# Kernel optimization log

Measured on AMD Instinct MI355X. Metric: run time of the kernel, lower is better.

## Reference

```python
import jax, jax.numpy as jnp
from jax import lax
import numpy as np

D_MODEL = 512
D_INNER = 1024   # expand=2 * d_model
D_STATE = 16
D_CONV = 4
DT_RANK = 32     # ceil(d_model/16)
B_SZ = 2
SEQ = 8192


def setup_inputs() -> dict:
    key = jax.random.key(0)
    ks = jax.random.split(key, 20)
    def n(k, shape, s=0.02):
        return jax.random.normal(k, shape, jnp.float32) * s
    inp = {
        "hidden_states": jax.random.normal(ks[0], (B_SZ, SEQ, D_MODEL), jnp.float32),
        "in_proj_w": n(ks[1], (2 * D_INNER, D_MODEL)),
        "out_proj_w": n(ks[2], (D_MODEL, D_INNER)),
    }
    for i, sfx in enumerate(["f", "r"]):
        b = 3 + i * 7
        inp[f"conv_w_{sfx}"] = n(ks[b], (D_INNER, 1, D_CONV), 0.1)
        inp[f"conv_b_{sfx}"] = n(ks[b + 1], (D_INNER,), 0.1)
        inp[f"xproj_w_{sfx}"] = n(ks[b + 2], (DT_RANK + 2 * D_STATE, D_INNER))
        inp[f"dtproj_w_{sfx}"] = n(ks[b + 3], (D_INNER, DT_RANK), 0.1)
        # softplus-inverse of dt_init ~0.01 (Mamba-style dt bias init)
        inp[f"dtproj_b_{sfx}"] = jnp.log(jnp.expm1(jnp.full((D_INNER,), 0.01, jnp.float32)))
        inp[f"A_log_{sfx}"] = jnp.log(jnp.tile(jnp.arange(1, D_STATE + 1, dtype=jnp.float32), (D_INNER, 1)))
        inp[f"D_{sfx}"] = jnp.ones((D_INNER,), jnp.float32)
    return inp


def _mamba(u, in_w, out_w, conv_w, conv_b, xproj_w, dt_w, dt_b, A_log, D_skip):
    # u: (B, L, D_MODEL)
    B, L, _ = u.shape
    xz = jnp.einsum('bld,ed->ble', u, in_w)          # (B, L, 2*D_INNER)
    x, z = jnp.split(xz, 2, axis=-1)
    # depthwise causal conv1d over time
    xt = lax.conv_general_dilated(
        x.transpose(0, 2, 1), conv_w, (1,), [(D_CONV - 1, 0)],
        dimension_numbers=('NCH', 'OIH', 'NCH'), feature_group_count=D_INNER)
    x = jax.nn.silu(xt.transpose(0, 2, 1) + conv_b)   # (B, L, D_INNER)
    # input-dependent dt, B, C
    xdbl = jnp.einsum('ble,fe->blf', x, xproj_w)      # (B, L, DT_RANK + 2*D_STATE)
    dt = xdbl[..., :DT_RANK]
    Bm = xdbl[..., DT_RANK:DT_RANK + D_STATE]         # (B, L, N)
    Cm = xdbl[..., DT_RANK + D_STATE:]                # (B, L, N)
    delta = jax.nn.softplus(jnp.einsum('blr,er->ble', dt, dt_w) + dt_b)  # (B, L, D_INNER)
    A = -jnp.exp(A_log)                               # (D_INNER, N)
    dA = jnp.exp(delta[..., None] * A)                # (B, L, D_INNER, N)
    dBu = delta[..., None] * Bm[:, :, None, :] * x[..., None]

    def step(h, inps):
        dA_t, dBu_t, C_t = inps
        h = dA_t * h + dBu_t                          # (B, D_INNER, N)
        return h, jnp.einsum('ben,bn->be', h, C_t)

    h0 = jnp.zeros((B, D_INNER, D_STATE), u.dtype)
    _, ys = lax.scan(step, h0, (dA.transpose(1, 0, 2, 3),
                                dBu.transpose(1, 0, 2, 3),
                                Cm.transpose(1, 0, 2)))
    y = ys.transpose(1, 0, 2) + x * D_skip            # (B, L, D_INNER)
    y = y * jax.nn.silu(z)
    return jnp.einsum('ble,de->bld', y, out_w)


def reference(hidden_states, in_proj_w, out_proj_w,
              conv_w_f, conv_b_f, xproj_w_f, dtproj_w_f, dtproj_b_f, A_log_f, D_f,
              conv_w_r, conv_b_r, xproj_w_r, dtproj_w_r, dtproj_b_r, A_log_r, D_r):
    out = _mamba(hidden_states, in_proj_w, out_proj_w,
                 conv_w_f, conv_b_f, xproj_w_f, dtproj_w_f, dtproj_b_f, A_log_f, D_f)
    out_rev = _mamba(hidden_states[:, ::-1], in_proj_w, out_proj_w,
                     conv_w_r, conv_b_r, xproj_w_r, dtproj_w_r, dtproj_b_r, A_log_r, D_r)[:, ::-1]
    return out + out_rev
```

## Files before the change

### kernel.cpp

```cpp
#include <hip/hip_runtime.h>
#include <hip/hip_bf16.h>
#include <math.h>

#define B_SZ 2
#define SEQ  8192
#define DM   512
#define DI   1024
#define DS   16
#define DTR  32
#define M_TOT (B_SZ*SEQ)
#define LOG2E 1.44269504088896f
#define NCHAN  (4*DI*DS)
#define NG     (4*DI)
#define CLT    8

typedef __attribute__((ext_vector_type(8))) short bf16x8;
typedef __attribute__((ext_vector_type(4))) float f32x4;
typedef __attribute__((ext_vector_type(2))) float f32x2;
typedef unsigned short u16;

__device__ __forceinline__ float bf2f(u16 u){
  union { unsigned u; float f; } v; v.u = ((unsigned)u) << 16; return v.f;
}
__device__ __forceinline__ u16 f2bf(float f){
  union { float f; unsigned u; } v; v.f = f;
  unsigned r = v.u + 0x7FFFu + ((v.u >> 16) & 1u);
  return (u16)(r >> 16);
}
__device__ __forceinline__ float silu_f(float x){ return x / (1.f + __expf(-x)); }
__device__ __forceinline__ float softplus_f(float x){
  return (x > 15.f) ? x : __logf(1.f + __expf(x));
}
__device__ __forceinline__ float fexp2(float x){ return __builtin_amdgcn_exp2f(x); }

__device__ __forceinline__ void dA_generic(float d, const float* A2, float* dAv){
  #pragma unroll
  for (int n = 0; n < DS; n++) dAv[n] = fexp2(A2[n] * d);
}

__global__ __launch_bounds__(256) void cvt_k(
    const float* __restrict__ s, u16* __restrict__ d)
{
  const size_t i = (size_t)blockIdx.x * 256 + threadIdx.x;
  const float4 a = ((const float4*)s)[i * 2];
  const float4 b = ((const float4*)s)[i * 2 + 1];
  union { uint4 v; u16 h[8]; } o;
  o.h[0] = f2bf(a.x); o.h[1] = f2bf(a.y); o.h[2] = f2bf(a.z); o.h[3] = f2bf(a.w);
  o.h[4] = f2bf(b.x); o.h[5] = f2bf(b.y); o.h[6] = f2bf(b.z); o.h[7] = f2bf(b.w);
  ((uint4*)d)[i] = o.v;
}

#define WU_INW  131072
#define WU_XW   8192
#define WU_DTW  4096
#define WU_OUTW 65536
#define WU_TOT  (WU_INW + 2*WU_XW + 2*WU_DTW + WU_OUTW)
__global__ __launch_bounds__(256) void cvtw_k(
    const float* __restrict__ inw, const float* __restrict__ xwf,
    const float* __restrict__ xwr, const float* __restrict__ dtwf,
    const float* __restrict__ dtwr, const float* __restrict__ outw,
    u16* __restrict__ dst)
{
  int i = blockIdx.x * 256 + threadIdx.x;
  const float* s;
  int base = 0;
  if (i < WU_INW) { s = inw; }
  else if ((i -= WU_INW) < WU_XW) { s = xwf; base = WU_INW; }
  else if ((i -= WU_XW) < WU_XW)  { s = xwr; base = WU_INW + WU_XW; }
  else if ((i -= WU_XW) < WU_DTW) { s = dtwf; base = WU_INW + 2*WU_XW; }
  else if ((i -= WU_DTW) < WU_DTW){ s = dtwr; base = WU_INW + 2*WU_XW + WU_DTW; }
  else { i -= WU_DTW; s = outw; base = WU_INW + 2*WU_XW + 2*WU_DTW; }
  const float4 a = ((const float4*)s)[i * 2];
  const float4 b = ((const float4*)s)[i * 2 + 1];
  union { uint4 v; u16 h[8]; } o;
  o.h[0] = f2bf(a.x); o.h[1] = f2bf(a.y); o.h[2] = f2bf(a.z); o.h[3] = f2bf(a.w);
  o.h[4] = f2bf(b.x); o.h[5] = f2bf(b.y); o.h[6] = f2bf(b.z); o.h[7] = f2bf(b.w);
  ((uint4*)(dst))[base + i] = o.v;
}

template<int BN, int BK, int EPI, bool DUAL>
__global__ __launch_bounds__(256) void gemm_k(
    const u16* __restrict__ Ap,  const u16* __restrict__ Ap2, int lda,
    const u16* __restrict__ Bw,  const u16* __restrict__ Bw2, int K,
    void* __restrict__ out0, void* __restrict__ out02,
    void* __restrict__ out1, void* __restrict__ out12,
    const float* __restrict__ bias, const float* __restrict__ bias2, int ldo)
{
  constexpr int BM = 128;
  constexpr int NSLOT = BK / 8;
  constexpr int RPI   = 512 / BK;
  __shared__ __align__(16) u16 As[BM * BK];
  __shared__ __align__(16) u16 Bs[BN * BK];
  const int tid  = threadIdx.x;
  const int lane = tid & 63, wid = tid >> 6;
  const int mt = blockIdx.x, nt = blockIdx.y;
  const int z  = DUAL ? blockIdx.z : 0;
  const u16* A = z ? Ap2 : Ap;
  const u16* W = z ? Bw2 : Bw;
  void* o0 = z ? out02 : out0;
  void* o1 = z ? out12 : out1;
  const float* bi = z ? bias2 : bias;

  constexpr int FM = (BN == 128) ? 4 : 2;
  const int wm = (BN == 128) ? ((wid >> 1) * 64) : (wid * 32);
  const int wn = (BN == 128) ? ((wid & 1) * 64) : 0;

  f32x4 acc[FM][4];
  #pragma unroll
  for (int i = 0; i < FM; i++)
    #pragma unroll
    for (int j = 0; j < 4; j++)
      acc[i][j] = (f32x4){0.f, 0.f, 0.f, 0.f};

  const int sr   = lane / NSLOT;
  const int slot = lane % NSLOT;
  const int skey = (BK == 32) ? ((sr >> 1) & 3) : (sr & 7);
  const int sc   = (slot ^ skey) * 8;

  for (int k0 = 0; k0 < K; k0 += BK) {
    #pragma unroll
    for (int j = 0; j < BM / RPI / 4; j++) {
      const int chunk = wid * (BM / RPI / 4) + j;
      const u16* src = A + (size_t)(mt * BM + chunk * RPI + sr) * lda + (k0 + sc);
      __builtin_amdgcn_global_load_lds(
          (const __attribute__((address_space(1))) void*)src,
          (__attribute__((address_space(3))) void*)(As + chunk * 512), 16, 0, 0);
    }
    #pragma unroll
    for (int j = 0; j < BN / RPI / 4; j++) {
      const int chunk = wid * (BN / RPI / 4) + j;
      const u16* src = W + (size_t)(nt * BN + chunk * RPI + sr) * K + (k0 + sc);
      __builtin_amdgcn_global_load_lds(
          (const __attribute__((address_space(1))) void*)src,
          (__attribute__((address_space(3))) void*)(Bs + chunk * 512), 16, 0, 0);
    }
    __syncthreads();

    const int row  = lane & 15;
    const int rkey = (BK == 32) ? ((row >> 1) & 3) : (row & 7);
    #pragma unroll
    for (int kh = 0; kh < BK / 32; kh++) {
      const int sl = (kh * 4 + (lane >> 4)) ^ rkey;
      bf16x8 af[FM], bfr[4];
      #pragma unroll
      for (int i = 0; i < FM; i++)
        af[i] = *(const bf16x8*)&As[(wm + i * 16 + row) * BK + sl * 8];
      #pragma unroll
      for (int j = 0; j < 4; j++)
        bfr[j] = *(const bf16x8*)&Bs[(wn + j * 16 + row) * BK + sl * 8];
      #pragma unroll
      for (int i = 0; i < FM; i++)
        #pragma unroll
        for (int j = 0; j < 4; j++)
          acc[i][j] = __builtin_amdgcn_mfma_f32_16x16x32_bf16(af[i], bfr[j], acc[i][j], 0, 0, 0);
    }
    __syncthreads();
  }

  const int rb4 = (lane >> 4) * 4, col = lane & 15;
  #pragma unroll
  for (int i = 0; i < FM; i++) {
    #pragma unroll
    for (int j = 0; j < 4; j++) {
      #pragma unroll
      for (int r = 0; r < 4; r++) {
        const int m = mt * BM + wm + i * 16 + rb4 + r;
        const int n = nt * BN + wn + j * 16 + col;
        const float v = acc[i][j][r];
        if (EPI == 0) {
          if (n < DI) ((u16*)o0)[(size_t)m * DI + n] = f2bf(v);
          else        ((u16*)out1)[(size_t)m * DI + (n - DI)] = f2bf(silu_f(v));
        } else if (EPI == 1) {
          ((u16*)o0)[(size_t)m * ldo + n] = f2bf(v);
          if (n >= 32) ((float*)o1)[(size_t)m * 32 + (n - 32)] = v;
        } else if (EPI == 2) {
          ((u16*)o0)[(size_t)m * ldo + n] = f2bf(softplus_f(v + bi[n]));
        } else {
          ((float*)o0)[(size_t)m * ldo + n] = v;
        }
      }
    }
  }
}

__global__ __launch_bounds__(256) void conv2_k(
    const u16* __restrict__ xpre,
    const float* __restrict__ wf, const float* __restrict__ bf_,
    const float* __restrict__ wr, const float* __restrict__ br_,
    u16* __restrict__ xf, u16* __restrict__ xr)
{
  const int tid  = threadIdx.x;
  const int et   = tid & 127;
  const int lsub = tid >> 7;
  const int e0 = et * 8;
  const int b  = blockIdx.y;
  const int l0 = (blockIdx.x * 2 + lsub) * CLT;
  const size_t base = (size_t)b * SEQ * DI + e0;

  float4 wf4[8], wr4[8];
  float  bfv[8], brv[8];
  #pragma unroll
  for (int j = 0; j < 8; j++) {
    wf4[j] = *(const float4*)(wf + (e0 + j) * 4);
    wr4[j] = *(const float4*)(wr + (e0 + j) * 4);
    bfv[j] = bf_[e0 + j];
    brv[j] = br_[e0 + j];
  }

  float c0[8], c1[8], c2[8];
  auto loadv = [&](int l, float* dst) {
    if (l < 0 || l >= SEQ) {
      #pragma unroll
      for (int j = 0; j < 8; j++) dst[j] = 0.f;
      return;
    }
    union { uint4 v; u16 s[8]; } t;
    t.v = *(const uint4*)(xpre + base + (size_t)l * DI);
    #pragma unroll
    for (int j = 0; j < 8; j++) dst[j] = bf2f(t.s[j]);
  };
  loadv(l0 - 3, c0); loadv(l0 - 2, c1); loadv(l0 - 1, c2);

  #pragma unroll
  for (int i = 0; i < CLT + 3; i++) {
    const int l = l0 + i;
    float cn[8];
    loadv(l, cn);
    if (i < CLT) {
      union { uint4 v; u16 s[8]; } o;
      #pragma unroll
      for (int j = 0; j < 8; j++) {
        const float v = bfv[j] + wf4[j].x * c0[j] + wf4[j].y * c1[j]
                               + wf4[j].z * c2[j] + wf4[j].w * cn[j];
        o.s[j] = f2bf(silu_f(v));
      }
      *(uint4*)(xf + base + (size_t)l * DI) = o.v;
    }
    if (i >= 3) {
      const int lr = l - 3;
      union { uint4 v; u16 s[8]; } o;
      #pragma unroll
      for (int j = 0; j < 8; j++) {
        const float v = brv[j] + wr4[j].w * c0[j] + wr4[j].z * c1[j]
                               + wr4[j].y * c2[j] + wr4[j].x * cn[j];
        o.s[j] = f2bf(silu_f(v));
      }
      *(uint4*)(xr + base + (size_t)(SEQ - 1 - lr) * DI) = o.v;
    }
    #pragma unroll
    for (int j = 0; j < 8; j++) { c0[j] = c1[j]; c1[j] = c2[j]; c2[j] = cn[j]; }
  }
}

__device__ __forceinline__ bool a_check(const float* Al, int e, float& A20){
  float A2[DS];
  #pragma unroll
  for (int n = 0; n < DS; n++) A2[n] = -__expf(Al[e * DS + n]) * LOG2E;
  A20 = A2[0];
  bool st = true;
  #pragma unroll
  for (int n = 1; n < DS; n++)
    st = st && (fabsf(A2[n] - (float)(n + 1) * A20) <= 1e-3f * fabsf(A2[n]));
  return st;
}

template<int CT_>
__global__ __launch_bounds__(128) void scanA2_k(
    const float* __restrict__ bcf, const float* __restrict__ bcr,
    const u16* __restrict__ xf_,   const u16* __restrict__ xr_,
    const float* __restrict__ Alf, const float* __restrict__ Alr,
    const u16* __restrict__ df_,   const u16* __restrict__ dr_,
    float* __restrict__ sumdP, float* __restrict__ bP)
{
  const int e = blockIdx.x * 128 + threadIdx.x;
  const int c = blockIdx.y;
  const int dir = blockIdx.z >> 1, b = blockIdx.z & 1;
  const float* bc = dir ? bcr : bcf;
  const u16* x    = dir ? xr_ : xf_;
  const float* Al = dir ? Alr : Alf;
  const u16* dpre = dir ? dr_ : df_;

  float A20;
  const bool structured = a_check(Al, e, A20);

  float sumd = 0.f;
  const size_t m0 = (size_t)b * SEQ + (size_t)c * CT_;
  const int g = (dir * 2 + b) * DI + e;
  const size_t cb = (size_t)c * NCHAN + (size_t)g * DS;

  if (structured) {
    f32x2 h2[8];
    #pragma unroll
    for (int k = 0; k < 8; k++) h2[k] = (f32x2){0.f, 0.f};
    #pragma unroll 2
    for (int t = 0; t < CT_; t++) {
      const size_t m = m0 + t;
      const float d  = bf2f(dpre[m * DI + e]);
      const float xv = bf2f(x[m * DI + e]);
      const float dbx = d * xv;
      sumd += d;
      const f32x4* bp = (const f32x4*)(bc + m * 32);
      const f32x4 b0 = bp[0], b1 = bp[1], b2 = bp[2], b3 = bp[3];
      const float q = fexp2(A20 * d), q2 = q * q, q4 = q2 * q2, q8 = q4 * q4;
      const f32x2 q2v = (f32x2){q2, q2}, q4v = (f32x2){q4, q4}, q8v = (f32x2){q8, q8};
      const f32x2 dbx2 = (f32x2){dbx, dbx};
      const f32x2 p0 = (f32x2){q, q2};
      const f32x2 p1 = p0 * q2v, p2 = p0 * q4v, p3 = p1 * q4v;
      const f32x2 p4 = p0 * q8v, p5 = p1 * q8v, p6 = p2 * q8v, p7 = p3 * q8v;
      h2[0] = p0 * h2[0] + dbx2 * (f32x2){b0[0], b0[1]};
      h2[1] = p1 * h2[1] + dbx2 * (f32x2){b0[2], b0[3]};
      h2[2] = p2 * h2[2] + dbx2 * (f32x2){b1[0], b1[1]};
      h2[3] = p3 * h2[3] + dbx2 * (f32x2){b1[2], b1[3]};
      h2[4] = p4 * h2[4] + dbx2 * (f32x2){b2[0], b2[1]};
      h2[5] = p5 * h2[5] + dbx2 * (f32x2){b2[2], b2[3]};
      h2[6] = p6 * h2[6] + dbx2 * (f32x2){b3[0], b3[1]};
      h2[7] = p7 * h2[7] + dbx2 * (f32x2){b3[2], b3[3]};
    }
    #pragma unroll
    for (int k = 0; k < 8; k++) *(f32x2*)&bP[cb + 2 * k] = h2[k];
  } else {
    float A2[DS], h[DS];
    #pragma unroll
    for (int n = 0; n < DS; n++) { A2[n] = -__expf(Al[e * DS + n]) * LOG2E; h[n] = 0.f; }
    for (int t = 0; t < CT_; t++) {
      const size_t m = m0 + t;
      const float d  = bf2f(dpre[m * DI + e]);
      const float xv = bf2f(x[m * DI + e]);
      const float dbx = d * xv;
      sumd += d;
      float dAv[DS];
      dA_generic(d, A2, dAv);
      #pragma unroll
      for (int n = 0; n < DS; n++)
        h[n] = dAv[n] * h[n] + dbx * bc[m * 32 + n];
    }
    #pragma unroll
    for (int n = 0; n < DS; n++) bP[cb + n] = h[n];
  }
  sumdP[(size_t)c * NG + g] = sumd;
}

__global__ __launch_bounds__(256) void scanB_k(
    const float* __restrict__ sumdP, float* __restrict__ bP,
    const float* __restrict__ Alog_f, const float* __restrict__ Alog_r, int nchunk)
{
  const int ch = blockIdx.x * 256 + threadIdx.x;
  const int g = ch >> 4, n = ch & 15;
  const int dir = g >> 11, e = g & (DI - 1);
  const float* Al = dir ? Alog_r : Alog_f;
  const float A2 = -__expf(Al[e * DS + n]) * LOG2E;
  float h = 0.f;
  for (int c = 0; c < nchunk; c++) {
    const float a = fexp2(A2 * sumdP[(size_t)c * NG + g]);
    const size_t i = (size_t)c * NCHAN + ch;
    const float bb = bP[i];
    bP[i] = h;
    h = a * h + bb;
  }
}

template<int CT_>
__global__ __launch_bounds__(128) void scanC2_k(
    const float* __restrict__ bcf, const float* __restrict__ bcr,
    const u16* __restrict__ xf_,   const u16* __restrict__ xr_,
    const float* __restrict__ Alf, const float* __restrict__ Alr,
    const u16* __restrict__ df_,   const u16* __restrict__ dr_,
    const float* __restrict__ Dskf, const float* __restrict__ Dskr,
    const float* __restrict__ hin,
    u16* __restrict__ yf, u16* __restrict__ yr)
{
  const int e = blockIdx.x * 128 + threadIdx.x;
  const int c = blockIdx.y;
  const int dir = blockIdx.z >> 1, b = blockIdx.z & 1;
  const float* bc = dir ? bcr : bcf;
  const u16* x    = dir ? xr_ : xf_;
  const float* Al = dir ? Alr : Alf;
  const u16* dpre = dir ? dr_ : df_;
  const float dskip = (dir ? Dskr : Dskf)[e];

  float A20;
  const bool structured = a_check(Al, e, A20);

  const int g = (dir * 2 + b) * DI + e;
  const size_t cb = (size_t)c * NCHAN + (size_t)g * DS;
  const size_t m0 = (size_t)b * SEQ + (size_t)c * CT_;

  if (structured) {
    f32x2 h2[8];
    #pragma unroll
    for (int k = 0; k < 8; k++) h2[k] = *(const f32x2*)&hin[cb + 2 * k];
    #pragma unroll 2
    for (int t = 0; t < CT_; t++) {
      const size_t m = m0 + t;
      const float d  = bf2f(dpre[m * DI + e]);
      const float xv = bf2f(x[m * DI + e]);
      const float dbx = d * xv;
      const f32x4* bp = (const f32x4*)(bc + m * 32);
      const f32x4 b0 = bp[0], b1 = bp[1], b2 = bp[2], b3 = bp[3];
      const f32x4 c0 = bp[4], c1 = bp[5], c2 = bp[6], c3 = bp[7];
      const float q = fexp2(A20 * d), q2 = q * q, q4 = q2 * q2, q8 = q4 * q4;
      const f32x2 q2v = (f32x2){q2, q2}, q4v = (f32x2){q4, q4}, q8v = (f32x2){q8, q8};
      const f32x2 dbx2 = (f32x2){dbx, dbx};
      const f32x2 p0 = (f32x2){q, q2};
      const f32x2 p1 = p0 * q2v, p2 = p0 * q4v, p3 = p1 * q4v;
      const f32x2 p4 = p0 * q8v, p5 = p1 * q8v, p6 = p2 * q8v, p7 = p3 * q8v;
      f32x2 y2 = (f32x2){0.f, 0.f};
      h2[0] = p0 * h2[0] + dbx2 * (f32x2){b0[0], b0[1]};  y2 = y2 + h2[0] * (f32x2){c0[0], c0[1]};
      h2[1] = p1 * h2[1] + dbx2 * (f32x2){b0[2], b0[3]};  y2 = y2 + h2[1] * (f32x2){c0[2], c0[3]};
      h2[2] = p2 * h2[2] + dbx2 * (f32x2){b1[0], b1[1]};  y2 = y2 + h2[2] * (f32x2){c1[0], c1[1]};
      h2[3] = p3 * h2[3] + dbx2 * (f32x2){b1[2], b1[3]};  y2 = y2 + h2[3] * (f32x2){c1[2], c1[3]};
      h2[4] = p4 * h2[4] + dbx2 * (f32x2){b2[0], b2[1]};  y2 = y2 + h2[4] * (f32x2){c2[0], c2[1]};
      h2[5] = p5 * h2[5] + dbx2 * (f32x2){b2[2], b2[3]};  y2 = y2 + h2[5] * (f32x2){c2[2], c2[3]};
      h2[6] = p6 * h2[6] + dbx2 * (f32x2){b3[0], b3[1]};  y2 = y2 + h2[6] * (f32x2){c3[0], c3[1]};
      h2[7] = p7 * h2[7] + dbx2 * (f32x2){b3[2], b3[3]};  y2 = y2 + h2[7] * (f32x2){c3[2], c3[3]};
      const float yout = (y2[0] + y2[1]) + xv * dskip;
      if (dir == 0) {
        yf[m * DI + e] = f2bf(yout);
      } else {
        const size_t mo = (size_t)b * SEQ + (SEQ - 1 - (c * CT_ + t));
        yr[mo * DI + e] = f2bf(yout);
      }
    }
  } else {
    float A2[DS], h[DS];
    #pragma unroll
    for (int n = 0; n < DS; n++) A2[n] = -__expf(Al[e * DS + n]) * LOG2E;
    #pragma unroll
    for (int n = 0; n < DS; n++) h[n] = hin[cb + n];
    for (int t = 0; t < CT_; t++) {
      const size_t m = m0 + t;
      const float d  = bf2f(dpre[m * DI + e]);
      const float xv = bf2f(x[m * DI + e]);
      const float dbx = d * xv;
      float dAv[DS];
      dA_generic(d, A2, dAv);
      float y = 0.f;
      #pragma unroll
      for (int n = 0; n < DS; n++) {
        h[n] = dAv[n] * h[n] + dbx * bc[m * 32 + n];
        y += h[n] * bc[m * 32 + 16 + n];
      }
      const float yout = y + xv * dskip;
      if (dir == 0) {
        yf[m * DI + e] = f2bf(yout);
      } else {
        const size_t mo = (size_t)b * SEQ + (SEQ - 1 - (c * CT_ + t));
        yr[mo * DI + e] = f2bf(yout);
      }
    }
  }
}

__global__ __launch_bounds__(256) void comb_k(
    u16* __restrict__ yfp, const u16* __restrict__ yrp, const u16* __restrict__ szp)
{
  const size_t i = ((size_t)blockIdx.x * 256 + threadIdx.x) * 8;
  union { uint4 v; u16 s[8]; } A, Bq, S, O;
  A.v  = *(const uint4*)(yfp + i);
  Bq.v = *(const uint4*)(yrp + i);
  S.v  = *(const uint4*)(szp + i);
  #pragma unroll
  for (int j = 0; j < 8; j++)
    O.s[j] = f2bf((bf2f(A.s[j]) + bf2f(Bq.s[j])) * bf2f(S.s[j]));
  *(uint4*)(yfp + i) = O.v;
}

__global__ __launch_bounds__(256) void scanA_k(
    const u16* __restrict__ xdblf_, const u16* __restrict__ xdblr_,
    const u16* __restrict__ xf_,    const u16* __restrict__ xr_,
    const float* __restrict__ Alf,  const float* __restrict__ Alr,
    const float* __restrict__ dtwf, const float* __restrict__ dtwr,
    const float* __restrict__ dtbf, const float* __restrict__ dtbr,
    float* __restrict__ sumdP, float* __restrict__ bP, int ct)
{
  const int e = blockIdx.x * 256 + threadIdx.x;
  const int c = blockIdx.y;
  const int dir = blockIdx.z >> 1, b = blockIdx.z & 1;
  const u16* xdbl = dir ? xdblr_ : xdblf_;
  const u16* x    = dir ? xr_ : xf_;
  const float* Al = dir ? Alr : Alf;

  float A2[DS], h[DS], dw[DTR];
  #pragma unroll
  for (int n = 0; n < DS; n++) { A2[n] = -__expf(Al[e * DS + n]) * LOG2E; h[n] = 0.f; }
  const float* dtw = dir ? dtwr : dtwf;
  #pragma unroll
  for (int r = 0; r < DTR; r += 4) {
    const float4 v = *(const float4*)(dtw + e * DTR + r);
    dw[r] = v.x; dw[r+1] = v.y; dw[r+2] = v.z; dw[r+3] = v.w;
  }
  const float bias = (dir ? dtbr : dtbf)[e];

  float sumd = 0.f;
  const size_t m0 = (size_t)b * SEQ + (size_t)c * ct;
  for (int t = 0; t < ct; t++) {
    const size_t m = m0 + t;
    union { uint4 v[4]; u16 s[32]; } DT;
    #pragma unroll
    for (int q = 0; q < 4; q++) DT.v[q] = ((const uint4*)(xdbl + m * 64))[q];
    float a0 = 0.f, a1 = 0.f, a2 = 0.f, a3 = 0.f;
    #pragma unroll
    for (int r = 0; r < DTR; r += 4) {
      a0 += bf2f(DT.s[r+0]) * dw[r+0];
      a1 += bf2f(DT.s[r+1]) * dw[r+1];
      a2 += bf2f(DT.s[r+2]) * dw[r+2];
      a3 += bf2f(DT.s[r+3]) * dw[r+3];
    }
    const float d = softplus_f(((a0 + a1) + (a2 + a3)) + bias);
    const float xv  = bf2f(x[m * DI + e]);
    const float dbx = d * xv;
    sumd += d;
    union { uint4 v[2]; u16 s[16]; } Bv;
    Bv.v[0] = ((const uint4*)(xdbl + m * 64 + 32))[0];
    Bv.v[1] = ((const uint4*)(xdbl + m * 64 + 32))[1];
    float dAv[DS];
    dA_generic(d, A2, dAv);
    #pragma unroll
    for (int n = 0; n < DS; n++)
      h[n] = dAv[n] * h[n] + dbx * bf2f(Bv.s[n]);
  }
  const int g = (dir * 2 + b) * DI + e;
  const size_t cb = (size_t)c * NCHAN + (size_t)g * DS;
  #pragma unroll
  for (int n = 0; n < DS; n++) bP[cb + n] = h[n];
  sumdP[(size_t)c * NG + g] = sumd;
}

template<int MODE>
__global__ __launch_bounds__(256) void scanC_k(
    const u16* __restrict__ xdblf_, const u16* __restrict__ xdblr_,
    const u16* __restrict__ xf_,    const u16* __restrict__ xr_,
    const float* __restrict__ Alf,  const float* __restrict__ Alr,
    const float* __restrict__ dtwf, const float* __restrict__ dtwr,
    const float* __restrict__ dtbf, const float* __restrict__ dtbr,
    const float* __restrict__ Dskf, const float* __restrict__ Dskr,
    const float* __restrict__ hin,
    u16* __restrict__ yf, u16* __restrict__ yr,
    const u16* __restrict__ szp, int ct)
{
  const int e = blockIdx.x * 256 + threadIdx.x;
  const int c = blockIdx.y;
  const int dir = (MODE == 2); const int b = blockIdx.z;
  const u16* xdbl = dir ? xdblr_ : xdblf_;
  const u16* x    = dir ? xr_ : xf_;
  const float* Al = dir ? Alr : Alf;
  const float dskip = (dir ? Dskr : Dskf)[e];

  float A2[DS], h[DS], dw[DTR];
  #pragma unroll
  for (int n = 0; n < DS; n++) A2[n] = -__expf(Al[e * DS + n]) * LOG2E;
  const float* dtw = dir ? dtwr : dtwf;
  #pragma unroll
  for (int r = 0; r < DTR; r += 4) {
    const float4 v = *(const float4*)(dtw + e * DTR + r);
    dw[r] = v.x; dw[r+1] = v.y; dw[r+2] = v.z; dw[r+3] = v.w;
  }
  const float bias = (dir ? dtbr : dtbf)[e];

  const int g = (dir * 2 + b) * DI + e;
  const size_t cb = (size_t)c * NCHAN + (size_t)g * DS;
  #pragma unroll
  for (int n = 0; n < DS; n++) h[n] = hin[cb + n];
  const size_t m0 = (size_t)b * SEQ + (size_t)c * ct;

  for (int t = 0; t < ct; t++) {
    const size_t m = m0 + t;
    union { uint4 v[4]; u16 s[32]; } BC;
    #pragma unroll
    for (int q = 0; q < 4; q++) BC.v[q] = ((const uint4*)(xdbl + m * 64 + 32))[q];
    union { uint4 v[4]; u16 s[32]; } DT;
    #pragma unroll
    for (int q = 0; q < 4; q++) DT.v[q] = ((const uint4*)(xdbl + m * 64))[q];
    float a0 = 0.f, a1 = 0.f, a2 = 0.f, a3 = 0.f;
    #pragma unroll
    for (int r = 0; r < DTR; r += 4) {
      a0 += bf2f(DT.s[r+0]) * dw[r+0];
      a1 += bf2f(DT.s[r+1]) * dw[r+1];
      a2 += bf2f(DT.s[r+2]) * dw[r+2];
      a3 += bf2f(DT.s[r+3]) * dw[r+3];
    }
    const float d = softplus_f(((a0 + a1) + (a2 + a3)) + bias);
    const float xv  = bf2f(x[m * DI + e]);
    const float dbx = d * xv;
    float dAv[DS];
    dA_generic(d, A2, dAv);
    float y = 0.f;
    #pragma unroll
    for (int n = 0; n < DS; n++) {
      h[n] = dAv[n] * h[n] + dbx * bf2f(BC.s[n]);
      y += h[n] * bf2f(BC.s[16 + n]);
    }
    const float yout = y + xv * dskip;
    if (MODE == 1) {
      yf[m * DI + e] = f2bf(yout);
    } else {
      const size_t mo = (size_t)b * SEQ + (SEQ - 1 - (c * ct + t));
      const size_t moi = mo * DI + e;
      yr[moi] = f2bf((bf2f(yf[moi]) + yout) * bf2f(szp[moi]));
    }
  }
}

extern "C" void kernel_launch(void* const* d_in, const int* in_sizes, int n_in,
                              void* d_out, int out_size, void* d_ws, size_t ws_size,
                              hipStream_t stream)
{
  (void)in_sizes; (void)n_in; (void)out_size;
  const float* u      = (const float*)d_in[0];
  const float* in_w   = (const float*)d_in[1];
  const float* out_w  = (const float*)d_in[2];
  const float* cw_f   = (const float*)d_in[3];
  const float* cb_f   = (const float*)d_in[4];
  const float* xw_f   = (const float*)d_in[5];
  const float* dtw_f  = (const float*)d_in[6];
  const float* dtb_f  = (const float*)d_in[7];
  const float* Alog_f = (const float*)d_in[8];
  const float* D_f    = (const float*)d_in[9];
  const float* cw_r   = (const float*)d_in[10];
  const float* cb_r   = (const float*)d_in[11];
  const float* xw_r   = (const float*)d_in[12];
  const float* dtw_r  = (const float*)d_in[13];
  const float* dtb_r  = (const float*)d_in[14];
  const float* Alog_r = (const float*)d_in[15];
  const float* D_r    = (const float*)d_in[16];

  const size_t mexe = (size_t)M_TOT * DI;
  const size_t bc_bytes = (size_t)M_TOT * 32 * 4;
  const size_t need_big =
      5 * (mexe * 2) + 2 * ((size_t)M_TOT * 64 * 2) + 2 * bc_bytes +
      (size_t)WU_TOT * 16 +
      (size_t)128 * NG * 4 + (size_t)128 * NCHAN * 4 + 64 * 256;
  const bool big = (ws_size >= need_big);
  const int nchunk = 64;
  const int ct = SEQ / nchunk;

  char* ws = (char*)d_ws;
  size_t off = 0;
  auto alloc = [&](size_t bytes) -> void* {
    void* p = ws + off;
    off += (bytes + 255) & ~(size_t)255;
    return p;
  };
  u16*   ubf   = (u16*)alloc(mexe * 2);
  u16*   xpre  = (u16*)alloc(mexe * 2);
  u16*   xf    = (u16*)alloc(mexe * 2);
  u16*   xr    = (u16*)alloc(mexe * 2);
  u16*   xdblf = (u16*)alloc((size_t)M_TOT * 64 * 2);
  u16*   xdblr = (u16*)alloc((size_t)M_TOT * 64 * 2);
  float* bc32f = (float*)alloc(bc_bytes);
  float* bc32r = (float*)alloc(bc_bytes);
  u16*   wbf   = (u16*)alloc((size_t)WU_TOT * 16);
  float* sumdP = (float*)alloc((size_t)128 * NG * 4);
  float* bP    = (float*)alloc((size_t)128 * NCHAN * 4);
  u16*   dr    = big ? (u16*)alloc(mexe * 2) : nullptr;
  u16*   df    = ubf;
  u16*   szb   = (u16*)d_out;

  u16* winb  = wbf;
  u16* xwbf  = wbf + (size_t)WU_INW * 8;
  u16* xwbr  = xwbf + (size_t)WU_XW * 8;
  u16* dtwbf = xwbr + (size_t)WU_XW * 8;
  u16* dtwbr = dtwbf + (size_t)WU_DTW * 8;
  u16* outwb = dtwbr + (size_t)WU_DTW * 8;

  dim3 blk(256);
  cvt_k<<<dim3((unsigned)((size_t)M_TOT * DM / 8 / 256)), blk, 0, stream>>>(u, ubf);
  cvtw_k<<<dim3(WU_TOT / 256), blk, 0, stream>>>(in_w, xw_f, xw_r, dtw_f, dtw_r, out_w, wbf);
  gemm_k<128, 64, 0, false><<<dim3(128, 16), blk, 0, stream>>>(
      ubf, nullptr, DM, winb, nullptr, DM, xpre, nullptr, szb, nullptr, nullptr, nullptr, 0);
  conv2_k<<<dim3(SEQ / (2 * CLT), B_SZ), blk, 0, stream>>>(
      xpre, cw_f, cb_f, cw_r, cb_r, xf, xr);
  gemm_k<64, 64, 1, true><<<dim3(128, 1, 2), blk, 0, stream>>>(
      xf, xr, DI, xwbf, xwbr, DI, xdblf, xdblr, bc32f, bc32r, nullptr, nullptr, 64);

  if (big) {
    gemm_k<128, 32, 2, true><<<dim3(128, 8, 2), blk, 0, stream>>>(
        xdblf, xdblr, 64, dtwbf, dtwbr, DTR, df, dr, nullptr, nullptr, dtb_f, dtb_r, DI);
    scanA2_k<128><<<dim3(8, nchunk, 4), dim3(128), 0, stream>>>(
        bc32f, bc32r, xf, xr, Alog_f, Alog_r, df, dr, sumdP, bP);
    scanB_k<<<dim3(NCHAN / 256), blk, 0, stream>>>(sumdP, bP, Alog_f, Alog_r, nchunk);
    scanC2_k<128><<<dim3(8, nchunk, 4), dim3(128), 0, stream>>>(
        bc32f, bc32r, xf, xr, Alog_f, Alog_r, df, dr, D_f, D_r, bP, xf, xpre);
    comb_k<<<dim3((unsigned)(mexe / 8 / 256)), blk, 0, stream>>>(xf, xpre, szb);
    gemm_k<128, 64, 3, false><<<dim3(128, 4), blk, 0, stream>>>(
        xf, nullptr, DI, outwb, nullptr, DI, d_out, nullptr, nullptr, nullptr, nullptr, nullptr, DM);
  } else {
    scanA_k<<<dim3(4, nchunk, 4), blk, 0, stream>>>(
        xdblf, xdblr, xf, xr, Alog_f, Alog_r, dtw_f, dtw_r, dtb_f, dtb_r,
        sumdP, bP, ct);
    scanB_k<<<dim3(NCHAN / 256), blk, 0, stream>>>(sumdP, bP, Alog_f, Alog_r, nchunk);
    scanC_k<1><<<dim3(4, nchunk, 2), blk, 0, stream>>>(
        xdblf, xdblr, xf, xr, Alog_f, Alog_r, dtw_f, dtw_r, dtb_f, dtb_r,
        D_f, D_r, bP, xf, nullptr, nullptr, ct);
    scanC_k<2><<<dim3(4, nchunk, 2), blk, 0, stream>>>(
        xdblf, xdblr, xf, xr, Alog_f, Alog_r, dtw_f, dtw_r, dtb_f, dtb_r,
        D_f, D_r, bP, xf, xpre, szb, ct);
    gemm_k<128, 64, 3, false><<<dim3(128, 4), blk, 0, stream>>>(
        xpre, nullptr, DI, outwb, nullptr, DI, d_out, nullptr, nullptr, nullptr, nullptr, nullptr, DM);
  }
}
```

Measured before the change: 353.7 us.

## Emit half-chunk scan states so final scan pass runs on finer chunks

The first scan pass still walks 128-step chunks but now also saves the partial state and delta sum at the midpoint. A new carry kernel turns these into exact starting states for 64-step sub-chunks. The final pass can then launch twice as many blocks over 64-step chunks for more parallelism, while the first pass keeps its 128-step grid. This costs extra writes for the midpoint state and sum, and hardcodes 64 chunks and a midpoint sumdP offset, which assumes the buffers are sized for that.

```diff
diff --git a/kernel.cpp b/kernel.cpp
--- a/kernel.cpp
+++ b/kernel.cpp
@@ -272,6 +272,7 @@
     const u16* __restrict__ df_,   const u16* __restrict__ dr_,
     float* __restrict__ sumdP, float* __restrict__ bP)
 {
+  constexpr int HF = CT_ / 2;
   const int e = blockIdx.x * 128 + threadIdx.x;
   const int c = blockIdx.y;
   const int dir = blockIdx.z >> 1, b = blockIdx.z & 1;
@@ -283,17 +284,17 @@
   float A20;
   const bool structured = a_check(Al, e, A20);
 
-  float sumd = 0.f;
+  float sumd = 0.f, sumdH = 0.f;
   const size_t m0 = (size_t)b * SEQ + (size_t)c * CT_;
   const int g = (dir * 2 + b) * DI + e;
-  const size_t cb = (size_t)c * NCHAN + (size_t)g * DS;
+  const size_t cb0 = (size_t)(2 * c)     * NCHAN + (size_t)g * DS;
+  const size_t cb1 = (size_t)(2 * c + 1) * NCHAN + (size_t)g * DS;
 
   if (structured) {
-    f32x2 h2[8];
+    f32x2 h2[8], hH[8];
     #pragma unroll
     for (int k = 0; k < 8; k++) h2[k] = (f32x2){0.f, 0.f};
-    #pragma unroll 2
-    for (int t = 0; t < CT_; t++) {
+    auto step = [&](int t) {
       const size_t m = m0 + t;
       const float d  = bf2f(dpre[m * DI + e]);
       const float xv = bf2f(x[m * DI + e]);
@@ -315,14 +316,24 @@
       h2[5] = p5 * h2[5] + dbx2 * (f32x2){b2[2], b2[3]};
       h2[6] = p6 * h2[6] + dbx2 * (f32x2){b3[0], b3[1]};
       h2[7] = p7 * h2[7] + dbx2 * (f32x2){b3[2], b3[3]};
-    }
-    #pragma unroll
-    for (int k = 0; k < 8; k++) *(f32x2*)&bP[cb + 2 * k] = h2[k];
+    };
+    #pragma unroll 2
+    for (int t = 0; t < HF; t++) step(t);
+    #pragma unroll
+    for (int k = 0; k < 8; k++) hH[k] = h2[k];
+    sumdH = sumd;
+    #pragma unroll 2
+    for (int t = HF; t < CT_; t++) step(t);
+    #pragma unroll
+    for (int k = 0; k < 8; k++) {
+      *(f32x2*)&bP[cb0 + 2 * k] = hH[k];
+      *(f32x2*)&bP[cb1 + 2 * k] = h2[k];
+    }
   } else {
-    float A2[DS], h[DS];
+    float A2[DS], h[DS], hH[DS];
     #pragma unroll
     for (int n = 0; n < DS; n++) { A2[n] = -__expf(Al[e * DS + n]) * LOG2E; h[n] = 0.f; }
-    for (int t = 0; t < CT_; t++) {
+    auto step = [&](int t) {
       const size_t m = m0 + t;
       const float d  = bf2f(dpre[m * DI + e]);
       const float xv = bf2f(x[m * DI + e]);
@@ -333,11 +344,42 @@
       #pragma unroll
       for (int n = 0; n < DS; n++)
         h[n] = dAv[n] * h[n] + dbx * bc[m * 32 + n];
-    }
-    #pragma unroll
-    for (int n = 0; n < DS; n++) bP[cb + n] = h[n];
-  }
-  sumdP[(size_t)c * NG + g] = sumd;
+    };
+    for (int t = 0; t < HF; t++) step(t);
+    #pragma unroll
+    for (int n = 0; n < DS; n++) hH[n] = h[n];
+    sumdH = sumd;
+    for (int t = HF; t < CT_; t++) step(t);
+    #pragma unroll
+    for (int n = 0; n < DS; n++) {
+      bP[cb0 + n] = hH[n];
+      bP[cb1 + n] = h[n];
+    }
+  }
+  sumdP[(size_t)c * NG + g]        = sumd;
+  sumdP[(size_t)(64 + c) * NG + g] = sumdH;
+}
+
+__global__ __launch_bounds__(256) void scanB2_k(
+    const float* __restrict__ sumdP, float* __restrict__ bP,
+    const float* __restrict__ Alog_f, const float* __restrict__ Alog_r)
+{
+  const int ch = blockIdx.x * 256 + threadIdx.x;
+  const int g = ch >> 4, n = ch & 15;
+  const int dir = g >> 11, e = g & (DI - 1);
+  const float* Al = dir ? Alog_r : Alog_f;
+  const float A2 = -__expf(Al[e * DS + n]) * LOG2E;
+  float h = 0.f;
+  for (int c = 0; c < 64; c++) {
+    const float sF = sumdP[(size_t)c * NG + g];
+    const float sH = sumdP[(size_t)(64 + c) * NG + g];
+    const size_t i0 = (size_t)(2 * c) * NCHAN + ch;
+    const size_t i1 = i0 + NCHAN;
+    const float cH = bP[i0], cF = bP[i1];
+    bP[i0] = h;
+    bP[i1] = fexp2(A2 * sH) * h + cH;
+    h = fexp2(A2 * sF) * h + cF;
+  }
 }
 
 __global__ __launch_bounds__(256) void scanB_k(
@@ -676,10 +718,10 @@
   if (big) {
     gemm_k<128, 32, 2, true><<<dim3(128, 8, 2), blk, 0, stream>>>(
         xdblf, xdblr, 64, dtwbf, dtwbr, DTR, df, dr, nullptr, nullptr, dtb_f, dtb_r, DI);
-    scanA2_k<128><<<dim3(8, nchunk, 4), dim3(128), 0, stream>>>(
+    scanA2_k<128><<<dim3(8, 64, 4), dim3(128), 0, stream>>>(
         bc32f, bc32r, xf, xr, Alog_f, Alog_r, df, dr, sumdP, bP);
-    scanB_k<<<dim3(NCHAN / 256), blk, 0, stream>>>(sumdP, bP, Alog_f, Alog_r, nchunk);
-    scanC2_k<128><<<dim3(8, nchunk, 4), dim3(128), 0, stream>>>(
+    scanB2_k<<<dim3(NCHAN / 256), blk, 0, stream>>>(sumdP, bP, Alog_f, Alog_r);
+    scanC2_k<64><<<dim3(8, 128, 4), dim3(128), 0, stream>>>(
         bc32f, bc32r, xf, xr, Alog_f, Alog_r, df, dr, D_f, D_r, bP, xf, xpre);
     comb_k<<<dim3((unsigned)(mexe / 8 / 256)), blk, 0, stream>>>(xf, xpre, szb);
     gemm_k<128, 64, 3, false><<<dim3(128, 4), blk, 0, stream>>>(
```

Measured after the change: 350.6 us. No clear change (-0.9%).
